# Performance work log

Measured on AMD Instinct MI355X. Metric: run time of the kernel, lower is better.

Reference implementation:

```python
import math
import jax, jax.numpy as jnp
import numpy as np

D = 1536      # d_model
H = 12        # n_heads
L = 12        # n_layers
V = 50257     # vocab (hardcoded in module)
P = 1024      # max positions (hardcoded)
B = 1         # batch (must be 1: pos-embed uses arange(len(idx)))
S = 1024      # sequence length


def setup_inputs() -> dict:
    key = jax.random.key(0)
    ks = jax.random.split(key, 10)
    sc = 0.02
    n = lambda k, shape: (jax.random.normal(k, shape, jnp.float32) * sc)
    return {
        "idx": jax.random.randint(ks[0], (B, S), 0, V),
        "mask": jnp.tril(jnp.ones((S, S), jnp.int32)),  # causal mask
        "tok_emb": n(ks[1], (V, D)),
        "pos_emb": n(ks[2], (P, D)),
        "Wqkv": n(ks[3], (L, D, 3 * D)), "bqkv": jnp.zeros((L, 3 * D), jnp.float32),
        "Wo":   n(ks[4], (L, D, D)),     "bo":   jnp.zeros((L, D), jnp.float32),
        "W1":   n(ks[5], (L, D, 4 * D)), "b1":   jnp.zeros((L, 4 * D), jnp.float32),
        "W2":   n(ks[6], (L, 4 * D, D)), "b2":   jnp.zeros((L, D), jnp.float32),
        "ln_g": jnp.ones((D,), jnp.float32), "ln_b": jnp.zeros((D,), jnp.float32),
        "Wout": n(ks[7], (D, D)), "bout": jnp.zeros((D,), jnp.float32),
    }


def _gpt_forward(idx, mask, tok_emb, pos_emb, Wqkv, bqkv, Wo, bo,
                 W1, b1, W2, b2, ln_g, ln_b, Wout, bout):
    b, s = idx.shape
    d = tok_emb.shape[1]
    hd = d // H
    scale = 1.0 / math.sqrt(d)  # note: module divides by sqrt(d_model), not head_dim

    # faithful quirk: position_embedding(arange(len(idx))) -> (B, D), broadcasts since B==1
    x = tok_emb[idx] + pos_emb[:b]  # (B,S,D)

    mask0 = (mask == 0)  # (S,S) -> broadcast over (B,H,S,S)

    def block(x, p):
        wqkv, bqkv_, wo, bo_, w1, b1_, w2, b2_ = p
        qkv = x @ wqkv + bqkv_                       # (B,S,3D)
        q, k, v = jnp.split(qkv, 3, axis=-1)
        q = q.reshape(b, s, H, hd)
        k = k.reshape(b, s, H, hd)
        v = v.reshape(b, s, H, hd)
        scores = jnp.einsum('bqhd,bkhd->bhqk', q, k) * scale
        scores = jnp.where(mask0, -jnp.inf, scores)
        attn = jax.nn.softmax(scores, axis=-2)       # non-standard: softmax over QUERY axis
        o = jnp.einsum('bhqk,bkhd->bqhd', attn, v).reshape(b, s, d)
        x = x + (o @ wo + bo_)                       # attention residual
        x = x + (jax.nn.relu(x @ w1 + b1_) @ w2 + b2_)  # FFN residual (on post-attn x)
        return x, None

    x, _ = jax.lax.scan(block, x, (Wqkv, bqkv, Wo, bo, W1, b1, W2, b2))

    # final LayerNorm (eps=1e-5 like torch default)
    mu = jnp.mean(x, axis=-1, keepdims=True)
    var = jnp.mean(jnp.square(x - mu), axis=-1, keepdims=True)
    xn = (x - mu) * jax.lax.rsqrt(var + 1e-5) * ln_g + ln_b
    return xn @ Wout + bout


def reference(idx, mask, tok_emb, pos_emb, Wqkv, bqkv, Wo, bo,
              W1, b1, W2, b2, ln_g, ln_b, Wout, bout):
    return _gpt_forward(idx, mask, tok_emb, pos_emb, Wqkv, bqkv, Wo, bo,
                        W1, b1, W2, b2, ln_g, ln_b, Wout, bout)
```

## Files before the change

### kernel.cpp

```cpp
#include <hip/hip_runtime.h>
#include <stdint.h>
#include <math.h>

#define D_MODEL 1536
#define NH 12
#define HD 128
#define NL 12
#define SEQ 1024
#define D3 4608
#define D4 6144
#define SCALE 0.025515518153991442f

typedef __attribute__((ext_vector_type(8))) short short8;
typedef __attribute__((ext_vector_type(4))) float floatx4;

__device__ __forceinline__ uint32_t packhi(float a, float b) {
  return (__float_as_uint(a) >> 16) | (__float_as_uint(b) & 0xFFFF0000u);
}
__device__ __forceinline__ float truncf32(float a) {
  return __uint_as_float(__float_as_uint(a) & 0xFFFF0000u);
}
__device__ __forceinline__ void split8v(float4 v0, float4 v1, uint4 &hi, uint4 &lo) {
  hi.x = packhi(v0.x, v0.y); hi.y = packhi(v0.z, v0.w);
  hi.z = packhi(v1.x, v1.y); hi.w = packhi(v1.z, v1.w);
  lo.x = packhi(v0.x - truncf32(v0.x), v0.y - truncf32(v0.y));
  lo.y = packhi(v0.z - truncf32(v0.z), v0.w - truncf32(v0.w));
  lo.z = packhi(v1.x - truncf32(v1.x), v1.y - truncf32(v1.y));
  lo.w = packhi(v1.z - truncf32(v1.z), v1.w - truncf32(v1.w));
}

__device__ __forceinline__ int xcd_chunk_id(int nwg) {
  int orig = blockIdx.x;
  int xcd = orig & 7, pos = orig >> 3;
  int q = nwg >> 3, r = nwg & 7;
  return (xcd < r ? xcd * (q + 1) : r * (q + 1) + (xcd - r) * q) + pos;
}

__global__ __launch_bounds__(256)
void embed_kernel(const int* __restrict__ idx, const float* __restrict__ tok,
                  const float* __restrict__ pos, float* __restrict__ x) {
  int i = blockIdx.x * 256 + threadIdx.x;
  int s = i / D_MODEL;
  int d = i - s * D_MODEL;
  x[i] = tok[(size_t)idx[s] * D_MODEL + d] + pos[d];
}

template<int BM, bool RELU, bool RES, int SPLITK, bool TA2>
__global__ __launch_bounds__(256)
void mgemm_kernel(const float* __restrict__ A, const float* __restrict__ Ab,
                  const float* __restrict__ B,
                  const float* __restrict__ bias, const float* __restrict__ res,
                  float* __restrict__ C, int M, int N, int K, int NC, int NR) {
  constexpr int MI = BM / 32;
  constexpr int AE = BM / 8;
  constexpr int TPR = 32 / AE;
  __shared__ short Ah[2][BM][36], Al[2][BM][36];
  __shared__ short Bh[2][128][36], Bl[2][128][36];
  const int tid = threadIdx.x;
  const int lane = tid & 63, wave = tid >> 6;

  const int lid = xcd_chunk_id(NC * NR * SPLITK);
  const int z   = lid / (NC * NR);
  const int rem = lid - z * (NC * NR);
  const int ct  = rem / NR;
  const int rt  = rem - ct * NR;
  const int bm = rt * BM, bn = ct << 7;

  const int wm = (wave >> 1) * (BM / 2), wn = (wave & 1) << 6;
  const int fr = lane & 15, fk = (lane >> 4) << 3;
  const int Kc = K / SPLITK;
  const int kbase = (SPLITK > 1) ? z * Kc : 0;

  floatx4 acc[MI][4];
#pragma unroll
  for (int i = 0; i < MI; i++)
#pragma unroll
    for (int j = 0; j < 4; j++) acc[i][j] = (floatx4){0.f, 0.f, 0.f, 0.f};

  const int ar = tid / TPR;
  const int ac = (tid % TPR) * AE;
  const int bc = tid & 127;
  const int bkq = (tid >> 7) << 4;
  const float* Ag  = A + (size_t)(bm + ar) * K + kbase + ac;
  const float* Ag2 = TA2 ? (Ab + (size_t)(bm + ar) * K + kbase + ac) : nullptr;
  const float* Bg = B + (size_t)(kbase + bkq) * N + bn + bc;

  float a_reg[AE];
  float b_reg[16];

  auto LOADG = [&](int k0) {
#pragma unroll
    for (int e = 0; e < AE / 4; e++) {
      float4 v = *(const float4*)(Ag + k0 + 4 * e);
      if constexpr (TA2) {
        float4 w = *(const float4*)(Ag2 + k0 + 4 * e);
        v.x += w.x; v.y += w.y; v.z += w.z; v.w += w.w;
      }
      a_reg[4 * e + 0] = v.x; a_reg[4 * e + 1] = v.y;
      a_reg[4 * e + 2] = v.z; a_reg[4 * e + 3] = v.w;
    }
    const float* Bp = Bg + (size_t)k0 * N;
#pragma unroll
    for (int j = 0; j < 16; j++) b_reg[j] = Bp[(size_t)j * N];
  };
  auto STORE = [&](int buf) {
#pragma unroll
    for (int e = 0; e < AE / 8; e++) {
      float4 v0 = {a_reg[8 * e + 0], a_reg[8 * e + 1], a_reg[8 * e + 2], a_reg[8 * e + 3]};
      float4 v1 = {a_reg[8 * e + 4], a_reg[8 * e + 5], a_reg[8 * e + 6], a_reg[8 * e + 7]};
      uint4 hi, lo; split8v(v0, v1, hi, lo);
      *(uint4*)&Ah[buf][ar][ac + 8 * e] = hi;
      *(uint4*)&Al[buf][ar][ac + 8 * e] = lo;
    }
#pragma unroll
    for (int e = 0; e < 2; e++) {
      float4 u0 = {b_reg[8 * e + 0], b_reg[8 * e + 1], b_reg[8 * e + 2], b_reg[8 * e + 3]};
      float4 u1 = {b_reg[8 * e + 4], b_reg[8 * e + 5], b_reg[8 * e + 6], b_reg[8 * e + 7]};
      uint4 hi, lo; split8v(u0, u1, hi, lo);
      *(uint4*)&Bh[buf][bc][bkq + 8 * e] = hi;
      *(uint4*)&Bl[buf][bc][bkq + 8 * e] = lo;
    }
  };

  LOADG(0);
  STORE(0);
  __syncthreads();

  for (int k0 = 0; k0 < Kc; k0 += 32) {
    const int cur = (k0 >> 5) & 1;
    const bool more = (k0 + 32 < Kc);
    if (more) LOADG(k0 + 32);

    short8 ah[MI], al[MI], bh[4], bl[4];
#pragma unroll
    for (int i = 0; i < MI; i++) {
      ah[i] = *(const short8*)&Ah[cur][wm + (i << 4) + fr][fk];
      al[i] = *(const short8*)&Al[cur][wm + (i << 4) + fr][fk];
    }
#pragma unroll
    for (int j = 0; j < 4; j++) {
      bh[j] = *(const short8*)&Bh[cur][wn + (j << 4) + fr][fk];
      bl[j] = *(const short8*)&Bl[cur][wn + (j << 4) + fr][fk];
    }
#pragma unroll
    for (int i = 0; i < MI; i++)
#pragma unroll
      for (int j = 0; j < 4; j++) {
        acc[i][j] = __builtin_amdgcn_mfma_f32_16x16x32_bf16(ah[i], bh[j], acc[i][j], 0, 0, 0);
        acc[i][j] = __builtin_amdgcn_mfma_f32_16x16x32_bf16(ah[i], bl[j], acc[i][j], 0, 0, 0);
        acc[i][j] = __builtin_amdgcn_mfma_f32_16x16x32_bf16(al[i], bh[j], acc[i][j], 0, 0, 0);
      }

    if (more) STORE(cur ^ 1);
    __syncthreads();
  }

  const int cr = (lane >> 4) << 2, cc = lane & 15;
  if constexpr (SPLITK > 1) {
    float* Cp = C + (size_t)z * M * N;
#pragma unroll
    for (int j = 0; j < 4; j++) {
      const int col = bn + wn + (j << 4) + cc;
#pragma unroll
      for (int i = 0; i < MI; i++) {
        const int row0 = bm + wm + (i << 4) + cr;
#pragma unroll
        for (int r = 0; r < 4; r++)
          Cp[(size_t)(row0 + r) * N + col] = acc[i][j][r];
      }
    }
  } else {
#pragma unroll
    for (int j = 0; j < 4; j++) {
      const int col = bn + wn + (j << 4) + cc;
      const float bv = bias[col];
#pragma unroll
      for (int i = 0; i < MI; i++) {
        const int row0 = bm + wm + (i << 4) + cr;
#pragma unroll
        for (int r = 0; r < 4; r++) {
          float v = acc[i][j][r] + bv;
          if constexpr (RES) v += res[(size_t)(row0 + r) * N + col];
          if constexpr (RELU) v = fmaxf(v, 0.f);
          C[(size_t)(row0 + r) * N + col] = v;
        }
      }
    }
  }
}

template<bool HASB, bool RES, bool RELU>
__global__ __launch_bounds__(256)
void combine_kernel(const float* __restrict__ p0, const float* __restrict__ p1,
                    const float* __restrict__ bias, const float* __restrict__ res,
                    float* __restrict__ C, int N) {
  const int i = (blockIdx.x * 256 + threadIdx.x) << 2;
  float4 a = *(const float4*)&p0[i];
  float4 b = *(const float4*)&p1[i];
  float4 r = {a.x + b.x, a.y + b.y, a.z + b.z, a.w + b.w};
  if constexpr (HASB) {
    const int col = i % N;
    float4 bv = *(const float4*)&bias[col];
    r.x += bv.x; r.y += bv.y; r.z += bv.z; r.w += bv.w;
  }
  if constexpr (RES) {
    float4 rv = *(const float4*)&res[i];
    r.x += rv.x; r.y += rv.y; r.z += rv.z; r.w += rv.w;
  }
  if constexpr (RELU) {
    r.x = fmaxf(r.x, 0.f); r.y = fmaxf(r.y, 0.f);
    r.z = fmaxf(r.z, 0.f); r.w = fmaxf(r.w, 0.f);
  }
  *(float4*)&C[i] = r;
}

__global__ __launch_bounds__(256)
void scores_kernel(const float* __restrict__ qkv, float* __restrict__ scores,
                   float* __restrict__ pstats) {
  __shared__ short Qh[128][40], Ql[128][40], Kh[128][40], Kl[128][40];
  const int tid = threadIdx.x;
  const int lane = tid & 63, wave = tid >> 6;

  const int lid = xcd_chunk_id(NH * 36);
  const int h = lid / 36;
  int t = lid - h * 36;
  int rr = 0;
  while ((rr + 1) * (rr + 2) / 2 <= t) rr++;
  const int bi = rr << 7;
  const int bj = (t - rr * (rr + 1) / 2) << 7;

  const int wm = (wave >> 1) << 6, wn = (wave & 1) << 6;
  const int fr = lane & 15, fk = (lane >> 4) << 3;
  const float* Q = qkv + h * HD;
  const float* Kp = qkv + D_MODEL + h * HD;

  floatx4 acc[4][4];
#pragma unroll
  for (int i = 0; i < 4; i++)
#pragma unroll
    for (int j = 0; j < 4; j++) acc[i][j] = (floatx4){0.f, 0.f, 0.f, 0.f};

  const int ar = tid >> 1;
  const int ac = (tid & 1) << 4;

  for (int k0 = 0; k0 < HD; k0 += 32) {
    __syncthreads();
    {
      const float* Qp = Q + (size_t)(bi + ar) * D3 + k0 + ac;
#pragma unroll
      for (int e = 0; e < 2; e++) {
        float4 v0 = *(const float4*)(Qp + 8 * e);
        float4 v1 = *(const float4*)(Qp + 8 * e + 4);
        uint4 hi, lo; split8v(v0, v1, hi, lo);
        *(uint4*)&Qh[ar][ac + 8 * e] = hi;
        *(uint4*)&Ql[ar][ac + 8 * e] = lo;
      }
      const float* Kpp = Kp + (size_t)(bj + ar) * D3 + k0 + ac;
#pragma unroll
      for (int e = 0; e < 2; e++) {
        float4 v0 = *(const float4*)(Kpp + 8 * e);
        float4 v1 = *(const float4*)(Kpp + 8 * e + 4);
        uint4 hi, lo; split8v(v0, v1, hi, lo);
        *(uint4*)&Kh[ar][ac + 8 * e] = hi;
        *(uint4*)&Kl[ar][ac + 8 * e] = lo;
      }
    }
    __syncthreads();
    short8 qh[4], ql[4], kh[4], kl[4];
#pragma unroll
    for (int i = 0; i < 4; i++) {
      qh[i] = *(const short8*)&Qh[wm + (i << 4) + fr][fk];
      ql[i] = *(const short8*)&Ql[wm + (i << 4) + fr][fk];
      kh[i] = *(const short8*)&Kh[wn + (i << 4) + fr][fk];
      kl[i] = *(const short8*)&Kl[wn + (i << 4) + fr][fk];
    }
#pragma unroll
    for (int i = 0; i < 4; i++)
#pragma unroll
      for (int j = 0; j < 4; j++) {
        acc[i][j] = __builtin_amdgcn_mfma_f32_16x16x32_bf16(qh[i], kh[j], acc[i][j], 0, 0, 0);
        acc[i][j] = __builtin_amdgcn_mfma_f32_16x16x32_bf16(qh[i], kl[j], acc[i][j], 0, 0, 0);
        acc[i][j] = __builtin_amdgcn_mfma_f32_16x16x32_bf16(ql[i], kh[j], acc[i][j], 0, 0, 0);
        acc[i][j] = __builtin_amdgcn_mfma_f32_16x16x32_bf16(ql[i], kl[j], acc[i][j], 0, 0, 0);
      }
  }

  const int cr = (lane >> 4) << 2, cc = lane & 15;
  float* S = scores + (size_t)h * SEQ * SEQ;
  const int qc = (bi >> 6) + (wave >> 1);
  float* Pm = pstats + (size_t)((h * 16 + qc) * 2 + 0) * 1024;
  float* Pz = pstats + (size_t)((h * 16 + qc) * 2 + 1) * 1024;
#pragma unroll
  for (int j = 0; j < 4; j++) {
    const int col = bj + wn + (j << 4) + cc;
    float vv[16];
    float m = -1e30f;
#pragma unroll
    for (int i = 0; i < 4; i++) {
      const int row0 = bi + wm + (i << 4) + cr;
#pragma unroll
      for (int r = 0; r < 4; r++) {
        float v = (col <= row0 + r) ? acc[i][j][r] * SCALE : -1e30f;
        S[(size_t)(row0 + r) * SEQ + col] = v;
        vv[i * 4 + r] = v;
        m = fmaxf(m, v);
      }
    }
    float zz = 0.f;
#pragma unroll
    for (int t2 = 0; t2 < 16; t2++) zz += __expf(vv[t2] - m);
    if (m == -1e30f) zz = 0.f;
#pragma unroll
    for (int off = 16; off <= 32; off <<= 1) {
      float mo = __shfl_xor(m, off, 64);
      float zo = __shfl_xor(zz, off, 64);
      float mn = fmaxf(m, mo);
      zz = zz * __expf(m - mn) + zo * __expf(mo - mn);
      m = mn;
    }
    if ((lane >> 4) == 0) { Pm[col] = m; Pz[col] = zz; }
  }
}

__global__ __launch_bounds__(256)
void colstatB_kernel(const float* __restrict__ pstats, float* __restrict__ stats) {
  const int i = blockIdx.x * 256 + threadIdx.x;
  const int h = i >> 10, c = i & 1023;
  const int q0 = c >> 6;
  float m = -1e30f;
  for (int qc = q0; qc < 16; qc++)
    m = fmaxf(m, pstats[(size_t)((h * 16 + qc) * 2 + 0) * 1024 + c]);
  float z = 0.f;
  for (int qc = q0; qc < 16; qc++) {
    float pm = pstats[(size_t)((h * 16 + qc) * 2 + 0) * 1024 + c];
    float pz = pstats[(size_t)((h * 16 + qc) * 2 + 1) * 1024 + c];
    z += pz * __expf(pm - m);
  }
  stats[h * 2048 + c] = m;
  stats[h * 2048 + 1024 + c] = 1.f / z;
}

__global__ __launch_bounds__(256)
void av_kernel(const float* __restrict__ qkv, const float* __restrict__ scores,
               const float* __restrict__ stats, float* __restrict__ part) {
  __shared__ short Ph[64][40], Pl[64][40], Vh[128][40], Vl[128][40];
  const int tid = threadIdx.x;
  const int lane = tid & 63, wave = tid >> 6;

  const int lid = xcd_chunk_id(NH * 32);
  const int h = lid >> 5;
  const int t = lid & 31;
  const int y = t >> 1, z = t & 1;
  const int bm = y << 6;

  const int wm = (wave >> 1) << 5, wn = (wave & 1) << 6;
  const int fr = lane & 15, fk = (lane >> 4) << 3;
  const float* S = scores + (size_t)h * SEQ * SEQ;
  const float* Mh = stats + h * 2048;
  const float* Rh = Mh + 1024;
  const float* V = qkv + 2 * D_MODEL + h * HD;

  floatx4 acc[2][4];
#pragma unroll
  for (int i = 0; i < 2; i++)
#pragma unroll
    for (int j = 0; j < 4; j++) acc[i][j] = (floatx4){0.f, 0.f, 0.f, 0.f};

  const int ar = tid >> 2;
  const int ac = (tid & 3) << 3;
  const int bc = tid & 127;
  const int bkq = (tid >> 7) << 4;

  const int kbeg = z * (y + 1) * 32;
  const int kend = (z + 1) * (y + 1) * 32;
  for (int k0 = kbeg; k0 < kend; k0 += 32) {
    __syncthreads();
    {
      const float* Sp = S + (size_t)(bm + ar) * SEQ + k0 + ac;
      float4 v0 = *(const float4*)(Sp);
      float4 v1 = *(const float4*)(Sp + 4);
      float t8[8] = {v0.x, v0.y, v0.z, v0.w, v1.x, v1.y, v1.z, v1.w};
      float4 p0, p1;
      {
        int kk = k0 + ac;
        p0.x = __expf(t8[0] - Mh[kk + 0]) * Rh[kk + 0];
        p0.y = __expf(t8[1] - Mh[kk + 1]) * Rh[kk + 1];
        p0.z = __expf(t8[2] - Mh[kk + 2]) * Rh[kk + 2];
        p0.w = __expf(t8[3] - Mh[kk + 3]) * Rh[kk + 3];
        p1.x = __expf(t8[4] - Mh[kk + 4]) * Rh[kk + 4];
        p1.y = __expf(t8[5] - Mh[kk + 5]) * Rh[kk + 5];
        p1.z = __expf(t8[6] - Mh[kk + 6]) * Rh[kk + 6];
        p1.w = __expf(t8[7] - Mh[kk + 7]) * Rh[kk + 7];
      }
      uint4 hi, lo; split8v(p0, p1, hi, lo);
      *(uint4*)&Ph[ar][ac] = hi;
      *(uint4*)&Pl[ar][ac] = lo;
    }
    {
      const float* Vp = V + (size_t)(k0 + bkq) * D3 + bc;
#pragma unroll
      for (int e = 0; e < 2; e++) {
        float4 u0, u1;
        u0.x = Vp[(size_t)(8 * e + 0) * D3]; u0.y = Vp[(size_t)(8 * e + 1) * D3];
        u0.z = Vp[(size_t)(8 * e + 2) * D3]; u0.w = Vp[(size_t)(8 * e + 3) * D3];
        u1.x = Vp[(size_t)(8 * e + 4) * D3]; u1.y = Vp[(size_t)(8 * e + 5) * D3];
        u1.z = Vp[(size_t)(8 * e + 6) * D3]; u1.w = Vp[(size_t)(8 * e + 7) * D3];
        uint4 hi, lo; split8v(u0, u1, hi, lo);
        *(uint4*)&Vh[bc][bkq + 8 * e] = hi;
        *(uint4*)&Vl[bc][bkq + 8 * e] = lo;
      }
    }
    __syncthreads();
    short8 ph[2], pl[2], vh[4], vl[4];
#pragma unroll
    for (int i = 0; i < 2; i++) {
      ph[i] = *(const short8*)&Ph[wm + (i << 4) + fr][fk];
      pl[i] = *(const short8*)&Pl[wm + (i << 4) + fr][fk];
    }
#pragma unroll
    for (int j = 0; j < 4; j++) {
      vh[j] = *(const short8*)&Vh[wn + (j << 4) + fr][fk];
      vl[j] = *(const short8*)&Vl[wn + (j << 4) + fr][fk];
    }
#pragma unroll
    for (int i = 0; i < 2; i++)
#pragma unroll
      for (int j = 0; j < 4; j++) {
        acc[i][j] = __builtin_amdgcn_mfma_f32_16x16x32_bf16(ph[i], vh[j], acc[i][j], 0, 0, 0);
        acc[i][j] = __builtin_amdgcn_mfma_f32_16x16x32_bf16(ph[i], vl[j], acc[i][j], 0, 0, 0);
        acc[i][j] = __builtin_amdgcn_mfma_f32_16x16x32_bf16(pl[i], vh[j], acc[i][j], 0, 0, 0);
      }
  }

  const int cr = (lane >> 4) << 2, cc = lane & 15;
  float* Cp = part + (size_t)z * SEQ * D_MODEL;
#pragma unroll
  for (int j = 0; j < 4; j++) {
    const int col = h * HD + wn + (j << 4) + cc;
#pragma unroll
    for (int i = 0; i < 2; i++) {
      const int row0 = bm + wm + (i << 4) + cr;
#pragma unroll
      for (int r = 0; r < 4; r++)
        Cp[(size_t)(row0 + r) * D_MODEL + col] = acc[i][j][r];
    }
  }
}

__global__ __launch_bounds__(256)
void ln_kernel(const float* __restrict__ x, const float* __restrict__ g,
               const float* __restrict__ bb, float* __restrict__ y) {
  __shared__ float red[8];
  const int row = blockIdx.x;
  const float* xr = x + (size_t)row * D_MODEL;
  float v[6];
  float s = 0.f, sq = 0.f;
#pragma unroll
  for (int i = 0; i < 6; i++) {
    v[i] = xr[256 * i + threadIdx.x];
    s += v[i];
    sq += v[i] * v[i];
  }
#pragma unroll
  for (int off = 32; off >= 1; off >>= 1) {
    s += __shfl_down(s, off, 64);
    sq += __shfl_down(sq, off, 64);
  }
  const int lane = threadIdx.x & 63, w = threadIdx.x >> 6;
  if (lane == 0) { red[w] = s; red[4 + w] = sq; }
  __syncthreads();
  if (threadIdx.x == 0) {
    red[0] = red[0] + red[1] + red[2] + red[3];
    red[4] = red[4] + red[5] + red[6] + red[7];
  }
  __syncthreads();
  const float mu = red[0] * (1.f / D_MODEL);
  const float var = red[4] * (1.f / D_MODEL) - mu * mu;
  const float rs = rsqrtf(var + 1e-5f);
#pragma unroll
  for (int i = 0; i < 6; i++) {
    int c = 256 * i + threadIdx.x;
    y[(size_t)row * D_MODEL + c] = (v[i] - mu) * rs * g[c] + bb[c];
  }
}

extern "C" void kernel_launch(void* const* d_in, const int* in_sizes, int n_in,
                              void* d_out, int out_size, void* d_ws, size_t ws_size,
                              hipStream_t stream) {
  (void)in_sizes; (void)n_in; (void)out_size; (void)ws_size;
  const int*   idx     = (const int*)d_in[0];
  const float* tok_emb = (const float*)d_in[2];
  const float* pos_emb = (const float*)d_in[3];
  const float* Wqkv    = (const float*)d_in[4];
  const float* bqkv    = (const float*)d_in[5];
  const float* Wo      = (const float*)d_in[6];
  const float* bo      = (const float*)d_in[7];
  const float* W1      = (const float*)d_in[8];
  const float* b1      = (const float*)d_in[9];
  const float* W2      = (const float*)d_in[10];
  const float* b2      = (const float*)d_in[11];
  const float* ln_g    = (const float*)d_in[12];
  const float* ln_b    = (const float*)d_in[13];
  const float* Wout    = (const float*)d_in[14];
  const float* bout    = (const float*)d_in[15];
  float* out = (float*)d_out;

  char* ws = (char*)d_ws;
  float* x      = (float*)(ws);
  float* qkv    = (float*)(ws + 6291456);
  float* stats  = (float*)(ws + 25165824);
  float* pstats = (float*)(ws + 25264128);
  float* part   = (float*)(ws + 26836992);
  float* U      = (float*)(ws + 52002816);
  float* scores = U;
  float* h1     = U;
  float* xn     = U;
  const size_t PN = (size_t)SEQ * D_MODEL;

  embed_kernel<<<6144, 256, 0, stream>>>(idx, tok_emb, pos_emb, x);

  for (int l = 0; l < NL; l++) {
    const float* wqkv = Wqkv + (size_t)l * D_MODEL * D3;
    const float* bq   = bqkv + (size_t)l * D3;
    const float* wo   = Wo   + (size_t)l * D_MODEL * D_MODEL;
    const float* bo_  = bo   + (size_t)l * D_MODEL;
    const float* w1   = W1   + (size_t)l * D_MODEL * D4;
    const float* b1_  = b1   + (size_t)l * D4;
    const float* w2   = W2   + (size_t)l * D4 * D_MODEL;
    const float* b2_  = b2   + (size_t)l * D_MODEL;

    mgemm_kernel<128, false, false, 1, false><<<288, 256, 0, stream>>>(
        x, nullptr, wqkv, bq, nullptr, qkv, SEQ, D3, D_MODEL, 36, 8);
    scores_kernel<<<432, 256, 0, stream>>>(qkv, scores, pstats);
    colstatB_kernel<<<48, 256, 0, stream>>>(pstats, stats);
    av_kernel<<<384, 256, 0, stream>>>(qkv, scores, stats, part);
    mgemm_kernel<64, false, false, 2, true><<<384, 256, 0, stream>>>(
        part, part + PN, wo, nullptr, nullptr, part + 2 * PN,
        SEQ, D_MODEL, D_MODEL, 12, 16);
    combine_kernel<true, true, false><<<1536, 256, 0, stream>>>(
        part + 2 * PN, part + 3 * PN, bo_, x, x, D_MODEL);
    mgemm_kernel<128, true, false, 1, false><<<384, 256, 0, stream>>>(
        x, nullptr, w1, b1_, nullptr, h1, SEQ, D4, D_MODEL, 48, 8);
    mgemm_kernel<64, false, false, 2, false><<<384, 256, 0, stream>>>(
        h1, nullptr, w2, nullptr, nullptr, part, SEQ, D_MODEL, D4, 12, 16);
    combine_kernel<true, true, false><<<1536, 256, 0, stream>>>(
        part, part + PN, b2_, x, x, D_MODEL);
  }

  ln_kernel<<<SEQ, 256, 0, stream>>>(x, ln_g, ln_b, xn);
  mgemm_kernel<64, false, false, 2, false><<<384, 256, 0, stream>>>(
      xn, nullptr, Wout, nullptr, nullptr, part, SEQ, D_MODEL, D_MODEL, 12, 16);
  combine_kernel<true, false, false><<<1536, 256, 0, stream>>>(
      part, part + PN, bout, nullptr, out, D_MODEL);
}
```

Baseline: 5.054 ms.

## Fuse attention-output combine into FFN1 A-load and colstats into AV kernel

The separate colstat kernel goes away: each AV block now computes its column softmax max and reciprocal sum into shared memory from the partial stats. The post-attention combine (split-K partials, bias, residual) is folded into the FFN1 GEMM's A-operand load, and one combine4 kernel builds the final residual update per layer. The QKV and FFN1 GEMMs switch from BM=128 to BM=64 tiles, doubling the grid. This saves launches and round trips to global memory, but the colstat work is repeated across blocks that share columns and the FFN1 A-loads read three tensors plus a bias.

```diff
diff --git a/kernel.cpp b/kernel.cpp
--- a/kernel.cpp
+++ b/kernel.cpp
@@ -45,9 +45,10 @@
   x[i] = tok[(size_t)idx[s] * D_MODEL + d] + pos[d];
 }
 
-template<int BM, bool RELU, bool RES, int SPLITK, bool TA2>
+template<int BM, bool RELU, bool RES, int SPLITK, int AMODE>
 __global__ __launch_bounds__(256)
 void mgemm_kernel(const float* __restrict__ A, const float* __restrict__ Ab,
+                  const float* __restrict__ Ac, const float* __restrict__ cbias,
                   const float* __restrict__ B,
                   const float* __restrict__ bias, const float* __restrict__ res,
                   float* __restrict__ C, int M, int N, int K, int NC, int NR) {
@@ -82,7 +83,9 @@
   const int bc = tid & 127;
   const int bkq = (tid >> 7) << 4;
   const float* Ag  = A + (size_t)(bm + ar) * K + kbase + ac;
-  const float* Ag2 = TA2 ? (Ab + (size_t)(bm + ar) * K + kbase + ac) : nullptr;
+  const float* Ag2 = (AMODE >= 1) ? (Ab + (size_t)(bm + ar) * K + kbase + ac) : nullptr;
+  const float* Ag3 = (AMODE >= 2) ? (Ac + (size_t)(bm + ar) * K + kbase + ac) : nullptr;
+  const float* CBg = (AMODE >= 2) ? (cbias + kbase + ac) : nullptr;
   const float* Bg = B + (size_t)(kbase + bkq) * N + bn + bc;
 
   float a_reg[AE];
@@ -92,9 +95,15 @@
 #pragma unroll
     for (int e = 0; e < AE / 4; e++) {
       float4 v = *(const float4*)(Ag + k0 + 4 * e);
-      if constexpr (TA2) {
+      if constexpr (AMODE >= 1) {
         float4 w = *(const float4*)(Ag2 + k0 + 4 * e);
         v.x += w.x; v.y += w.y; v.z += w.z; v.w += w.w;
+      }
+      if constexpr (AMODE >= 2) {
+        float4 u = *(const float4*)(Ag3 + k0 + 4 * e);
+        v.x += u.x; v.y += u.y; v.z += u.z; v.w += u.w;
+        float4 cb = *(const float4*)(CBg + k0 + 4 * e);
+        v.x += cb.x; v.y += cb.y; v.z += cb.z; v.w += cb.w;
       }
       a_reg[4 * e + 0] = v.x; a_reg[4 * e + 1] = v.y;
       a_reg[4 * e + 2] = v.z; a_reg[4 * e + 3] = v.w;
@@ -189,29 +198,38 @@
   }
 }
 
-template<bool HASB, bool RES, bool RELU>
-__global__ __launch_bounds__(256)
-void combine_kernel(const float* __restrict__ p0, const float* __restrict__ p1,
-                    const float* __restrict__ bias, const float* __restrict__ res,
-                    float* __restrict__ C, int N) {
+__global__ __launch_bounds__(256)
+void combine2_kernel(const float* __restrict__ p0, const float* __restrict__ p1,
+                     const float* __restrict__ bias, float* __restrict__ C, int N) {
   const int i = (blockIdx.x * 256 + threadIdx.x) << 2;
   float4 a = *(const float4*)&p0[i];
   float4 b = *(const float4*)&p1[i];
-  float4 r = {a.x + b.x, a.y + b.y, a.z + b.z, a.w + b.w};
-  if constexpr (HASB) {
-    const int col = i % N;
-    float4 bv = *(const float4*)&bias[col];
-    r.x += bv.x; r.y += bv.y; r.z += bv.z; r.w += bv.w;
-  }
-  if constexpr (RES) {
-    float4 rv = *(const float4*)&res[i];
-    r.x += rv.x; r.y += rv.y; r.z += rv.z; r.w += rv.w;
-  }
-  if constexpr (RELU) {
-    r.x = fmaxf(r.x, 0.f); r.y = fmaxf(r.y, 0.f);
-    r.z = fmaxf(r.z, 0.f); r.w = fmaxf(r.w, 0.f);
-  }
+  const int col = i % N;
+  float4 bv = *(const float4*)&bias[col];
+  float4 r = {a.x + b.x + bv.x, a.y + b.y + bv.y, a.z + b.z + bv.z, a.w + b.w + bv.w};
   *(float4*)&C[i] = r;
+}
+
+__global__ __launch_bounds__(256)
+void combine4_kernel(const float* __restrict__ x, const float* __restrict__ p2,
+                     const float* __restrict__ p3, const float* __restrict__ f0,
+                     const float* __restrict__ f1, const float* __restrict__ bo,
+                     const float* __restrict__ b2, float* __restrict__ xo) {
+  const int i = (blockIdx.x * 256 + threadIdx.x) << 2;
+  const int col = i % D_MODEL;
+  float4 vx = *(const float4*)&x[i];
+  float4 a = *(const float4*)&p2[i];
+  float4 b = *(const float4*)&p3[i];
+  float4 c = *(const float4*)&f0[i];
+  float4 d = *(const float4*)&f1[i];
+  float4 vo = *(const float4*)&bo[col];
+  float4 v2 = *(const float4*)&b2[col];
+  float4 r;
+  r.x = ((((vx.x + a.x) + b.x) + vo.x) + c.x) + d.x + v2.x;
+  r.y = ((((vx.y + a.y) + b.y) + vo.y) + c.y) + d.y + v2.y;
+  r.z = ((((vx.z + a.z) + b.z) + vo.z) + c.z) + d.z + v2.z;
+  r.w = ((((vx.w + a.w) + b.w) + vo.w) + c.w) + d.w + v2.w;
+  *(float4*)&xo[i] = r;
 }
 
 __global__ __launch_bounds__(256)
@@ -323,27 +341,10 @@
 }
 
 __global__ __launch_bounds__(256)
-void colstatB_kernel(const float* __restrict__ pstats, float* __restrict__ stats) {
-  const int i = blockIdx.x * 256 + threadIdx.x;
-  const int h = i >> 10, c = i & 1023;
-  const int q0 = c >> 6;
-  float m = -1e30f;
-  for (int qc = q0; qc < 16; qc++)
-    m = fmaxf(m, pstats[(size_t)((h * 16 + qc) * 2 + 0) * 1024 + c]);
-  float z = 0.f;
-  for (int qc = q0; qc < 16; qc++) {
-    float pm = pstats[(size_t)((h * 16 + qc) * 2 + 0) * 1024 + c];
-    float pz = pstats[(size_t)((h * 16 + qc) * 2 + 1) * 1024 + c];
-    z += pz * __expf(pm - m);
-  }
-  stats[h * 2048 + c] = m;
-  stats[h * 2048 + 1024 + c] = 1.f / z;
-}
-
-__global__ __launch_bounds__(256)
 void av_kernel(const float* __restrict__ qkv, const float* __restrict__ scores,
-               const float* __restrict__ stats, float* __restrict__ part) {
+               const float* __restrict__ pstats, float* __restrict__ part) {
   __shared__ short Ph[64][40], Pl[64][40], Vh[128][40], Vl[128][40];
+  __shared__ float Ms[512], Rs[512];
   const int tid = threadIdx.x;
   const int lane = tid & 63, wave = tid >> 6;
 
@@ -356,9 +357,27 @@
   const int wm = (wave >> 1) << 5, wn = (wave & 1) << 6;
   const int fr = lane & 15, fk = (lane >> 4) << 3;
   const float* S = scores + (size_t)h * SEQ * SEQ;
-  const float* Mh = stats + h * 2048;
-  const float* Rh = Mh + 1024;
   const float* V = qkv + 2 * D_MODEL + h * HD;
+
+  const int kbeg = z * (y + 1) * 32;
+  const int kend = (z + 1) * (y + 1) * 32;
+  const int ncols = kend - kbeg;
+
+  for (int c0 = tid; c0 < ncols; c0 += 256) {
+    const int c = kbeg + c0;
+    const int q0 = c >> 6;
+    float m = -1e30f;
+    for (int qc = q0; qc < 16; qc++)
+      m = fmaxf(m, pstats[(size_t)((h * 16 + qc) * 2 + 0) * 1024 + c]);
+    float zz = 0.f;
+    for (int qc = q0; qc < 16; qc++) {
+      float pm = pstats[(size_t)((h * 16 + qc) * 2 + 0) * 1024 + c];
+      float pz = pstats[(size_t)((h * 16 + qc) * 2 + 1) * 1024 + c];
+      zz += pz * __expf(pm - m);
+    }
+    Ms[c0] = m;
+    Rs[c0] = 1.f / zz;
+  }
 
   floatx4 acc[2][4];
 #pragma unroll
@@ -371,8 +390,6 @@
   const int bc = tid & 127;
   const int bkq = (tid >> 7) << 4;
 
-  const int kbeg = z * (y + 1) * 32;
-  const int kend = (z + 1) * (y + 1) * 32;
   for (int k0 = kbeg; k0 < kend; k0 += 32) {
     __syncthreads();
     {
@@ -382,15 +399,15 @@
       float t8[8] = {v0.x, v0.y, v0.z, v0.w, v1.x, v1.y, v1.z, v1.w};
       float4 p0, p1;
       {
-        int kk = k0 + ac;
-        p0.x = __expf(t8[0] - Mh[kk + 0]) * Rh[kk + 0];
-        p0.y = __expf(t8[1] - Mh[kk + 1]) * Rh[kk + 1];
-        p0.z = __expf(t8[2] - Mh[kk + 2]) * Rh[kk + 2];
-        p0.w = __expf(t8[3] - Mh[kk + 3]) * Rh[kk + 3];
-        p1.x = __expf(t8[4] - Mh[kk + 4]) * Rh[kk + 4];
-        p1.y = __expf(t8[5] - Mh[kk + 5]) * Rh[kk + 5];
-        p1.z = __expf(t8[6] - Mh[kk + 6]) * Rh[kk + 6];
-        p1.w = __expf(t8[7] - Mh[kk + 7]) * Rh[kk + 7];
+        int kk = k0 - kbeg + ac;
+        p0.x = __expf(t8[0] - Ms[kk + 0]) * Rs[kk + 0];
+        p0.y = __expf(t8[1] - Ms[kk + 1]) * Rs[kk + 1];
+        p0.z = __expf(t8[2] - Ms[kk + 2]) * Rs[kk + 2];
+        p0.w = __expf(t8[3] - Ms[kk + 3]) * Rs[kk + 3];
+        p1.x = __expf(t8[4] - Ms[kk + 4]) * Rs[kk + 4];
+        p1.y = __expf(t8[5] - Ms[kk + 5]) * Rs[kk + 5];
+        p1.z = __expf(t8[6] - Ms[kk + 6]) * Rs[kk + 6];
+        p1.w = __expf(t8[7] - Ms[kk + 7]) * Rs[kk + 7];
       }
       uint4 hi, lo; split8v(p0, p1, hi, lo);
       *(uint4*)&Ph[ar][ac] = hi;
@@ -508,8 +525,7 @@
   char* ws = (char*)d_ws;
   float* x      = (float*)(ws);
   float* qkv    = (float*)(ws + 6291456);
-  float* stats  = (float*)(ws + 25165824);
-  float* pstats = (float*)(ws + 25264128);
+  float* pstats = (float*)(ws + 25165824);
   float* part   = (float*)(ws + 26836992);
   float* U      = (float*)(ws + 52002816);
   float* scores = U;
@@ -529,27 +545,27 @@
     const float* w2   = W2   + (size_t)l * D4 * D_MODEL;
     const float* b2_  = b2   + (size_t)l * D_MODEL;
 
-    mgemm_kernel<128, false, false, 1, false><<<288, 256, 0, stream>>>(
-        x, nullptr, wqkv, bq, nullptr, qkv, SEQ, D3, D_MODEL, 36, 8);
+    mgemm_kernel<64, false, false, 1, 0><<<576, 256, 0, stream>>>(
+        x, nullptr, nullptr, nullptr, wqkv, bq, nullptr, qkv,
+        SEQ, D3, D_MODEL, 36, 16);
     scores_kernel<<<432, 256, 0, stream>>>(qkv, scores, pstats);
-    colstatB_kernel<<<48, 256, 0, stream>>>(pstats, stats);
-    av_kernel<<<384, 256, 0, stream>>>(qkv, scores, stats, part);
-    mgemm_kernel<64, false, false, 2, true><<<384, 256, 0, stream>>>(
-        part, part + PN, wo, nullptr, nullptr, part + 2 * PN,
+    av_kernel<<<384, 256, 0, stream>>>(qkv, scores, pstats, part);
+    mgemm_kernel<64, false, false, 2, 1><<<384, 256, 0, stream>>>(
+        part, part + PN, nullptr, nullptr, wo, nullptr, nullptr, part + 2 * PN,
         SEQ, D_MODEL, D_MODEL, 12, 16);
-    combine_kernel<true, true, false><<<1536, 256, 0, stream>>>(
-        part + 2 * PN, part + 3 * PN, bo_, x, x, D_MODEL);
-    mgemm_kernel<128, true, false, 1, false><<<384, 256, 0, stream>>>(
-        x, nullptr, w1, b1_, nullptr, h1, SEQ, D4, D_MODEL, 48, 8);
-    mgemm_kernel<64, false, false, 2, false><<<384, 256, 0, stream>>>(
-        h1, nullptr, w2, nullptr, nullptr, part, SEQ, D_MODEL, D4, 12, 16);
-    combine_kernel<true, true, false><<<1536, 256, 0, stream>>>(
-        part, part + PN, b2_, x, x, D_MODEL);
+    mgemm_kernel<64, true, false, 1, 2><<<768, 256, 0, stream>>>(
+        x, part + 2 * PN, part + 3 * PN, bo_, w1, b1_, nullptr, h1,
+        SEQ, D4, D_MODEL, 48, 16);
+    mgemm_kernel<64, false, false, 2, 0><<<384, 256, 0, stream>>>(
+        h1, nullptr, nullptr, nullptr, w2, nullptr, nullptr, part,
+        SEQ, D_MODEL, D4, 12, 16);
+    combine4_kernel<<<1536, 256, 0, stream>>>(
+        x, part + 2 * PN, part + 3 * PN, part, part + PN, bo_, b2_, x);
   }
 
   ln_kernel<<<SEQ, 256, 0, stream>>>(x, ln_g, ln_b, xn);
-  mgemm_kernel<64, false, false, 2, false><<<384, 256, 0, stream>>>(
-      xn, nullptr, Wout, nullptr, nullptr, part, SEQ, D_MODEL, D_MODEL, 12, 16);
-  combine_kernel<true, false, false><<<1536, 256, 0, stream>>>(
-      part, part + PN, bout, nullptr, out, D_MODEL);
-}
+  mgemm_kernel<64, false, false, 2, 0><<<384, 256, 0, stream>>>(
+      xn, nullptr, nullptr, nullptr, Wout, nullptr, nullptr, part,
+      SEQ, D_MODEL, D_MODEL, 12, 16);
+  combine2_kernel<<<1536, 256, 0, stream>>>(part, part + PN, bout, out, D_MODEL);
+}
```

Result: slower. 5.821 ms (+15.2%).
